# Kernel tuning notes

Hardware: AMD Instinct MI355X
Metric: run time of the kernel (lower is better)

Reference implementation:

```python
import jax, jax.numpy as jnp
import numpy as np

N = 100000          # total nodes
E = 1600000         # total edges
B = 500             # graphs in batch
NODES_PER_GRAPH = N // B
D_X, D_XDA = 96, 32
IN = D_X + D_XDA    # 128
HID = 128
OUT = 128


def setup_inputs() -> dict:
    key = jax.random.key(0)
    ks = jax.random.split(key, 12)
    s = 0.05
    x = jax.random.normal(ks[0], (N, D_X), jnp.float32)
    x_da = jax.random.normal(ks[1], (N, D_XDA), jnp.float32)
    edge_index = jax.random.randint(ks[2], (2, E), 0, N, jnp.int32).astype(jnp.int64)
    batch = (jnp.arange(N, dtype=jnp.int64) // NODES_PER_GRAPH)
    rootindex = jnp.arange(B, dtype=jnp.int64) * NODES_PER_GRAPH
    return {
        'x': x, 'x_da': x_da, 'edge_index': edge_index,
        'batch': batch, 'rootindex': rootindex,
        'td_w1': jax.random.normal(ks[3], (IN, HID), jnp.float32) * s,
        'td_b1': jnp.zeros((HID,), jnp.float32),
        'td_w2': jax.random.normal(ks[4], (HID + IN, OUT), jnp.float32) * s,
        'td_b2': jnp.zeros((OUT,), jnp.float32),
        'bu_w1': jax.random.normal(ks[5], (IN, HID), jnp.float32) * s,
        'bu_b1': jnp.zeros((HID,), jnp.float32),
        'bu_w2': jax.random.normal(ks[6], (HID + IN, OUT), jnp.float32) * s,
        'bu_b2': jnp.zeros((OUT,), jnp.float32),
        'mlp_w1': jax.random.normal(ks[7], ((OUT + HID) * 2, 2 * HID), jnp.float32) * s,
        'mlp_b1': jnp.zeros((2 * HID,), jnp.float32),
        'mlp_w2': jax.random.normal(ks[8], (2 * HID, 2), jnp.float32) * s,
        'mlp_b2': jnp.zeros((2,), jnp.float32),
    }


def gcn_conv(h, src, dst, W, b):
    # PyG GCNConv: h' = D^{-1/2} (A + I) D^{-1/2} (h W) + b,
    # messages flow src -> dst, deg counts incoming edges + self loop.
    h = h @ W                                              # [N, out]
    deg = jax.ops.segment_sum(jnp.ones((src.shape[0],), h.dtype), dst,
                              num_segments=N) + 1.0        # self loop
    dinv = jax.lax.rsqrt(deg)                              # deg >= 1
    norm = dinv[src] * dinv[dst]                           # [E]
    agg = jax.ops.segment_sum(h[src] * norm[:, None], dst, num_segments=N)
    agg = agg + h * (dinv * dinv)[:, None]                 # self-loop term
    return agg + b


def branch(x0, src, dst, w1, b1, w2, b2, batch, rootindex):
    # x0: [N, IN] = cat(x, x_da)
    x1 = x0
    h = gcn_conv(x0, src, dst, w1, b1)                     # [N, HID]
    x2 = h
    root1 = x1[rootindex[batch]]                           # root-extend gather
    h = jax.nn.relu(jnp.concatenate([h, root1], axis=1))   # dropout off (eval)
    h = jax.nn.relu(gcn_conv(h, src, dst, w2, b2))         # [N, OUT]
    root2 = x2[rootindex[batch]]
    h = jnp.concatenate([h, root2], axis=1)                # [N, OUT+HID]
    # scatter_mean over graphs
    sums = jax.ops.segment_sum(h, batch, num_segments=B)
    cnt = jax.ops.segment_sum(jnp.ones((N,), h.dtype), batch, num_segments=B)
    return sums / cnt[:, None]                             # [B, OUT+HID]


def reference(x, x_da, edge_index, batch, rootindex,
              td_w1, td_b1, td_w2, td_b2,
              bu_w1, bu_b1, bu_w2, bu_b2,
              mlp_w1, mlp_b1, mlp_w2, mlp_b2):
    x0 = jnp.concatenate([x, x_da], axis=1)                # [N, IN]
    src, dst = edge_index[0], edge_index[1]
    td = branch(x0, src, dst, td_w1, td_b1, td_w2, td_b2, batch, rootindex)
    bu = branch(x0, dst, src, bu_w1, bu_b1, bu_w2, bu_b2, batch, rootindex)
    g = jnp.concatenate([bu, td], axis=1)                  # [B, 4*HID]
    h = jax.nn.relu(g @ mlp_w1 + mlp_b1)
    return h @ mlp_w2 + mlp_b2                             # [B, 2]
```

## Files before the change

kernel.cpp:

```cpp
#include <hip/hip_runtime.h>

#define NN 100000
#define NE 1600000
#define NB 500
#define NPG 200
#define BS 128
#define NBUK 782
#define SLAB 2560
#define EPB2 4096
#define NEB2 391
#define NBLK 1563

typedef unsigned short ushortT;
typedef __attribute__((ext_vector_type(8))) short bf16x8;
typedef __attribute__((ext_vector_type(4))) float f32x4;

#define MFMA16(a, b, c) __builtin_amdgcn_mfma_f32_16x16x32_bf16(a, b, c, 0, 0, 0)

__device__ inline ushortT f2bf(float f) {
    unsigned u = __float_as_uint(f);
    return (ushortT)((u + 0x7FFF + ((u >> 16) & 1)) >> 16);
}
__device__ inline float bf2f(ushortT u) { return __uint_as_float((unsigned)u << 16); }
__device__ inline void addbf2(float& a0, float& a1, unsigned w) {
    a0 += __uint_as_float(w << 16);
    a1 += __uint_as_float(w & 0xFFFF0000u);
}
__device__ inline void addbf8(float* acc, uint4 w) {
    addbf2(acc[0], acc[1], w.x);
    addbf2(acc[2], acc[3], w.y);
    addbf2(acc[4], acc[5], w.z);
    addbf2(acc[6], acc[7], w.w);
}
__device__ inline bf16x8 cvt8(float4 f0, float4 f1) {
    bf16x8 r;
    r[0] = (short)f2bf(f0.x); r[1] = (short)f2bf(f0.y);
    r[2] = (short)f2bf(f0.z); r[3] = (short)f2bf(f0.w);
    r[4] = (short)f2bf(f1.x); r[5] = (short)f2bf(f1.y);
    r[6] = (short)f2bf(f1.z); r[7] = (short)f2bf(f1.w);
    return r;
}
__device__ inline bf16x8 relu_bf8(uint4 w) {
    bf16x8 r;
    unsigned ws[4] = {w.x, w.y, w.z, w.w};
#pragma unroll
    for (int i = 0; i < 4; i++) {
        unsigned v = ws[i];
        unsigned lo = (v & 0x8000u) ? 0u : (v & 0xFFFFu);
        unsigned hi = (v & 0x80000000u) ? 0u : (v & 0xFFFF0000u);
        r[2 * i]     = (short)lo;
        r[2 * i + 1] = (short)(hi >> 16);
    }
    return r;
}

__global__ void wprep_k(const float* __restrict__ w0, const float* __restrict__ w1,
                        const float* __restrict__ w2, const float* __restrict__ w3,
                        ushortT* __restrict__ wt) {
    int m = blockIdx.x >> 6;
    const float* w = (m == 0) ? w0 : (m == 1) ? w1 : (m == 2) ? w2 : w3;
    ushortT* o = wt + m * 16384;
    int idx = (blockIdx.x & 63) * 256 + threadIdx.x;
    int n = idx >> 7, k = idx & 127;
    o[idx] = f2bf(w[k * 128 + n]);
}

__global__ __launch_bounds__(512) void stage_slab_k(const int* __restrict__ ei,
                                                    int* __restrict__ bcnt_td,
                                                    int* __restrict__ bcnt_bu,
                                                    int* __restrict__ st_td,
                                                    int* __restrict__ st_bu) {
    __shared__ int h0[NBUK], h1[NBUK];
    const int t = threadIdx.x;
    for (int i = t; i < NBUK; i += 512) { h0[i] = 0; h1[i] = 0; }
    __syncthreads();
    int base = blockIdx.x * EPB2;
    int a[EPB2 / 512], b[EPB2 / 512];
#pragma unroll
    for (int j = 0; j < EPB2 / 512; j++) {
        int e = base + t + j * 512;
        a[j] = -1;
        if (e < NE) {
            a[j] = ei[e]; b[j] = ei[NE + e];
            atomicAdd(&h0[b[j] >> 7], 1);
            atomicAdd(&h1[a[j] >> 7], 1);
        }
    }
    __syncthreads();
    for (int i = t; i < NBUK; i += 512) {
        int c0 = h0[i], c1 = h1[i];
        if (c0) h0[i] = atomicAdd(&bcnt_td[i], c0);
        if (c1) h1[i] = atomicAdd(&bcnt_bu[i], c1);
    }
    __syncthreads();
#pragma unroll
    for (int j = 0; j < EPB2 / 512; j++) {
        if (a[j] >= 0) {
            int bk0 = b[j] >> 7;
            int o0 = atomicAdd(&h0[bk0], 1);
            st_td[bk0 * SLAB + o0] = (a[j] << 7) | (b[j] & 127);
            int bk1 = a[j] >> 7;
            int o1 = atomicAdd(&h1[bk1], 1);
            st_bu[bk1 * SLAB + o1] = (b[j] << 7) | (a[j] & 127);
        }
    }
}

__global__ __launch_bounds__(1024) void bscan_k(
    const int* __restrict__ c0, const int* __restrict__ c1,
    int* __restrict__ b0, int* __restrict__ b1) {
    const int* c = blockIdx.x ? c1 : c0;
    int* bb = blockIdx.x ? b1 : b0;
    __shared__ int sh[1024];
    const int t = threadIdx.x;
    int v = (t < NBUK) ? c[t] : 0;
    sh[t] = v;
    __syncthreads();
#pragma unroll
    for (int off = 1; off < 1024; off <<= 1) {
        int add = (t >= off) ? sh[t - off] : 0;
        __syncthreads();
        sh[t] += add;
        __syncthreads();
    }
    int excl = sh[t] - v;
    if (t < NBUK) bb[t] = excl;
    if (t == NBUK - 1) bb[NBUK] = sh[t];
}

__global__ __launch_bounds__(256) void place2_k(
    const int* __restrict__ st_td, const int* __restrict__ st_bu,
    const int* __restrict__ bcnt_td, const int* __restrict__ bcnt_bu,
    const int* __restrict__ bb_td, const int* __restrict__ bb_bu,
    int* __restrict__ rp_td, int* __restrict__ rp_bu,
    int* __restrict__ csr_td, int* __restrict__ csr_bu,
    float* __restrict__ dinv_td, float* __restrict__ dinv_bu) {
    const int dir = blockIdx.x >= NBUK;
    const int bucket = dir ? blockIdx.x - NBUK : blockIdx.x;
    const int* stage = (dir ? st_bu : st_td) + bucket * SLAB;
    const int n = (dir ? bcnt_bu : bcnt_td)[bucket];
    const int obase = (dir ? bb_bu : bb_td)[bucket];
    int* rp = dir ? rp_bu : rp_td;
    int* csr = dir ? csr_bu : csr_td;
    float* dinv = dir ? dinv_bu : dinv_td;

    const int node0 = bucket << 7;
    __shared__ int lcnt[BS], lsc[BS], lcur[BS];
    const int t = threadIdx.x;
    if (t < BS) lcnt[t] = 0;
    __syncthreads();
    for (int i = t; i < n; i += 256) atomicAdd(&lcnt[stage[i] & 127], 1);
    __syncthreads();
    if (t < BS) lsc[t] = lcnt[t];
    __syncthreads();
#pragma unroll
    for (int off = 1; off < BS; off <<= 1) {
        int add = (t < BS && t >= off) ? lsc[t - off] : 0;
        __syncthreads();
        if (t < BS) lsc[t] += add;
        __syncthreads();
    }
    if (t < BS) {
        int excl = lsc[t] - lcnt[t];
        lcur[t] = obase + excl;
        int node = node0 + t;
        if (node < NN) {
            rp[node] = obase + excl;
            dinv[node] = rsqrtf((float)(lcnt[t] + 1));
        }
    }
    if (bucket == NBUK - 1 && t == 0) rp[NN] = obase + n;
    __syncthreads();
    for (int i = t; i < n; i += 256) {
        int s = stage[i];
        int off = atomicAdd(&lcur[s & 127], 1);
        csr[off] = (int)((unsigned)s >> 7);
    }
}

__global__ __launch_bounds__(256) void gemm1x_k(
    const float* __restrict__ x, const float* __restrict__ xda,
    const ushortT* __restrict__ WTa, const ushortT* __restrict__ WTb,
    const float* __restrict__ dinv_a, const float* __restrict__ dinv_b,
    ushortT* __restrict__ hs_a, ushortT* __restrict__ hs_b) {
    const int t = threadIdx.x;
    const int wv = t >> 6, l = t & 63, lr = l & 15, lk = l >> 4;
    const int row0 = blockIdx.x * 64;
    const int cb0 = (wv * 2) * 16, cb1 = (wv * 2 + 1) * 16;

    bf16x8 bfr[2][2][4];
#pragma unroll
    for (int br = 0; br < 2; br++) {
        const ushortT* WT = br ? WTb : WTa;
#pragma unroll
        for (int c = 0; c < 2; c++) {
            const ushortT* base = WT + (size_t)((wv * 2 + c) * 16 + lr) * 128 + lk * 8;
#pragma unroll
            for (int kk = 0; kk < 4; kk++)
                bfr[br][c][kk] = *reinterpret_cast<const bf16x8*>(base + kk * 32);
        }
    }

#pragma unroll
    for (int rt = 0; rt < 4; rt++) {
        const int rtbase = row0 + rt * 16;
        int arow = rtbase + lr; if (arow >= NN) arow = NN - 1;
        bf16x8 af[4];
#pragma unroll
        for (int kk = 0; kk < 4; kk++) {
            int c8 = kk * 4 + lk;
            float4 f0, f1;
            if (c8 < 12) {
                const float* p = x + (size_t)arow * 96 + c8 * 8;
                f0 = *(const float4*)p; f1 = *(const float4*)(p + 4);
            } else {
                const float* p = xda + (size_t)arow * 32 + (c8 - 12) * 8;
                f0 = *(const float4*)p; f1 = *(const float4*)(p + 4);
            }
            af[kk] = cvt8(f0, f1);
        }
        f32x4 a00 = {0,0,0,0}, a01 = {0,0,0,0}, a10 = {0,0,0,0}, a11 = {0,0,0,0};
#pragma unroll
        for (int kk = 0; kk < 4; kk++) {
            a00 = MFMA16(af[kk], bfr[0][0][kk], a00);
            a01 = MFMA16(af[kk], bfr[0][1][kk], a01);
            a10 = MFMA16(af[kk], bfr[1][0][kk], a10);
            a11 = MFMA16(af[kk], bfr[1][1][kk], a11);
        }
        const int srow = rtbase + lk * 4;
        float4 da = *(const float4*)(dinv_a + srow);
        float4 db = *(const float4*)(dinv_b + srow);
        const float* dap = (const float*)&da;
        const float* dbp = (const float*)&db;
#pragma unroll
        for (int e = 0; e < 4; e++) {
            int r = srow + e;
            if (r < NN) {
                size_t ro = (size_t)r * 128;
                hs_a[ro + cb0 + lr] = f2bf(a00[e] * dap[e]);
                hs_a[ro + cb1 + lr] = f2bf(a01[e] * dap[e]);
                hs_b[ro + cb0 + lr] = f2bf(a10[e] * dbp[e]);
                hs_b[ro + cb1 + lr] = f2bf(a11[e] * dbp[e]);
            }
        }
    }
}

__global__ __launch_bounds__(256) void gemm2x_k(
    const ushortT* __restrict__ agg_a, const ushortT* __restrict__ agg_b,
    const ushortT* __restrict__ WTa, const ushortT* __restrict__ WTb,
    const float* __restrict__ rm_a, const float* __restrict__ rm_b,
    const float* __restrict__ dinv_a, const float* __restrict__ dinv_b,
    ushortT* __restrict__ hs_a, ushortT* __restrict__ hs_b) {
    const int brn = blockIdx.x >= NBLK;
    const ushortT* agg = brn ? agg_b : agg_a;
    const ushortT* WT  = brn ? WTb : WTa;
    const float* rm    = brn ? rm_b : rm_a;
    const float* dinv  = brn ? dinv_b : dinv_a;
    ushortT* hs        = brn ? hs_b : hs_a;
    const int blk = brn ? blockIdx.x - NBLK : blockIdx.x;
    const int t = threadIdx.x;
    const int wv = t >> 6, l = t & 63, lr = l & 15, lk = l >> 4;
    const int row0 = blk * 64;
    const int cb0 = (wv * 2) * 16, cb1 = (wv * 2 + 1) * 16;

    bf16x8 bfr[2][4];
#pragma unroll
    for (int c = 0; c < 2; c++) {
        const ushortT* base = WT + (size_t)((wv * 2 + c) * 16 + lr) * 128 + lk * 8;
#pragma unroll
        for (int kk = 0; kk < 4; kk++)
            bfr[c][kk] = *reinterpret_cast<const bf16x8*>(base + kk * 32);
    }

#pragma unroll
    for (int rt = 0; rt < 4; rt++) {
        const int rtbase = row0 + rt * 16;
        int arow = rtbase + lr; if (arow >= NN) arow = NN - 1;
        const ushortT* ap = agg + (size_t)arow * 128 + lk * 8;
        bf16x8 af[4];
#pragma unroll
        for (int kk = 0; kk < 4; kk++)
            af[kk] = relu_bf8(*reinterpret_cast<const uint4*>(ap + kk * 32));
        f32x4 a0 = {0,0,0,0}, a1 = {0,0,0,0};
#pragma unroll
        for (int kk = 0; kk < 4; kk++) {
            a0 = MFMA16(af[kk], bfr[0][kk], a0);
            a1 = MFMA16(af[kk], bfr[1][kk], a1);
        }
        const int srow = rtbase + lk * 4;
        float4 dv = *(const float4*)(dinv + srow);
        const float* dvp = (const float*)&dv;
#pragma unroll
        for (int e = 0; e < 4; e++) {
            int r = srow + e;
            if (r < NN) {
                int bg = r / NPG;
                size_t ro = (size_t)r * 128;
                float r0 = rm[(size_t)bg * 128 + cb0 + lr];
                float r1 = rm[(size_t)bg * 128 + cb1 + lr];
                hs[ro + cb0 + lr] = f2bf((a0[e] + r0) * dvp[e]);
                hs[ro + cb1 + lr] = f2bf((a1[e] + r1) * dvp[e]);
            }
        }
    }
}

template <int MODE>
__global__ __launch_bounds__(256) void gather16_k(
    const int* __restrict__ rp_a, const int* __restrict__ csr_a,
    const float* __restrict__ dinv_a, const ushortT* __restrict__ hs_a,
    const float* __restrict__ bias_a,
    const int* __restrict__ rp_b, const int* __restrict__ csr_b,
    const float* __restrict__ dinv_b, const ushortT* __restrict__ hs_b,
    const float* __restrict__ bias_b,
    ushortT* __restrict__ out_a, ushortT* __restrict__ out_b) {
    int v = blockIdx.x * 16 + (threadIdx.x >> 4);
    if (v >= NN) return;
    const int lane = threadIdx.x & 15;
    int ba = rp_a[v], ea = rp_a[v + 1];
    int bb = rp_b[v], eb = rp_b[v + 1];
    float acc_a[8], acc_b[8];
#pragma unroll
    for (int k = 0; k < 8; k++) { acc_a[k] = 0.f; acc_b[k] = 0.f; }
    addbf8(acc_a, *(const uint4*)(hs_a + (size_t)v * 128 + lane * 8));
    addbf8(acc_b, *(const uint4*)(hs_b + (size_t)v * 128 + lane * 8));

    while (ba < ea || bb < eb) {
        int na = ea - ba; if (na > 16) na = 16; if (na < 0) na = 0;
        int nb = eb - bb; if (nb > 16) nb = 16; if (nb < 0) nb = 0;
        int ia = (lane < na) ? csr_a[ba + lane] : 0;
        int ib = (lane < nb) ? csr_b[bb + lane] : 0;
#pragma unroll
        for (int i = 0; i < 16; i += 8) {
            if (i >= na && i >= nb) break;
            uint4 ua[8], ub[8];
            if (i < na) {
#pragma unroll
                for (int j = 0; j < 8; j++) {
                    int s = __shfl(ia, i + j, 16);
                    ua[j] = *(const uint4*)(hs_a + (size_t)s * 128 + lane * 8);
                }
            }
            if (i < nb) {
#pragma unroll
                for (int j = 0; j < 8; j++) {
                    int s = __shfl(ib, i + j, 16);
                    ub[j] = *(const uint4*)(hs_b + (size_t)s * 128 + lane * 8);
                }
            }
            if (i < na) {
#pragma unroll
                for (int j = 0; j < 8; j++)
                    if (i + j < na) addbf8(acc_a, ua[j]);
            }
            if (i < nb) {
#pragma unroll
                for (int j = 0; j < 8; j++)
                    if (i + j < nb) addbf8(acc_b, ub[j]);
            }
        }
        ba += 16; bb += 16;
    }

    float da = dinv_a[v], db = dinv_b[v];
    float4 pa0 = *(const float4*)(bias_a + lane * 8);
    float4 pa1 = *(const float4*)(bias_a + lane * 8 + 4);
    float4 pb0 = *(const float4*)(bias_b + lane * 8);
    float4 pb1 = *(const float4*)(bias_b + lane * 8 + 4);
    float oa[8], ob[8];
    const float* pap = (const float*)&pa0;
    oa[0] = fmaf(acc_a[0], da, pa0.x); oa[1] = fmaf(acc_a[1], da, pa0.y);
    oa[2] = fmaf(acc_a[2], da, pa0.z); oa[3] = fmaf(acc_a[3], da, pa0.w);
    oa[4] = fmaf(acc_a[4], da, pa1.x); oa[5] = fmaf(acc_a[5], da, pa1.y);
    oa[6] = fmaf(acc_a[6], da, pa1.z); oa[7] = fmaf(acc_a[7], da, pa1.w);
    ob[0] = fmaf(acc_b[0], db, pb0.x); ob[1] = fmaf(acc_b[1], db, pb0.y);
    ob[2] = fmaf(acc_b[2], db, pb0.z); ob[3] = fmaf(acc_b[3], db, pb0.w);
    ob[4] = fmaf(acc_b[4], db, pb1.x); ob[5] = fmaf(acc_b[5], db, pb1.y);
    ob[6] = fmaf(acc_b[6], db, pb1.z); ob[7] = fmaf(acc_b[7], db, pb1.w);
    (void)pap;
    if (MODE == 1) {
#pragma unroll
        for (int k = 0; k < 8; k++) { oa[k] = fmaxf(oa[k], 0.f); ob[k] = fmaxf(ob[k], 0.f); }
    }
    uint4 wa, wb;
    wa.x = (unsigned)f2bf(oa[0]) | ((unsigned)f2bf(oa[1]) << 16);
    wa.y = (unsigned)f2bf(oa[2]) | ((unsigned)f2bf(oa[3]) << 16);
    wa.z = (unsigned)f2bf(oa[4]) | ((unsigned)f2bf(oa[5]) << 16);
    wa.w = (unsigned)f2bf(oa[6]) | ((unsigned)f2bf(oa[7]) << 16);
    wb.x = (unsigned)f2bf(ob[0]) | ((unsigned)f2bf(ob[1]) << 16);
    wb.y = (unsigned)f2bf(ob[2]) | ((unsigned)f2bf(ob[3]) << 16);
    wb.z = (unsigned)f2bf(ob[4]) | ((unsigned)f2bf(ob[5]) << 16);
    wb.w = (unsigned)f2bf(ob[6]) | ((unsigned)f2bf(ob[7]) << 16);
    *(uint4*)(out_a + (size_t)v * 128 + lane * 8) = wa;
    *(uint4*)(out_b + (size_t)v * 128 + lane * 8) = wb;
}

__global__ void roots_k(
    const float* __restrict__ x, const float* __restrict__ xda,
    const int* __restrict__ root,
    const ushortT* __restrict__ agg_a, const ushortT* __restrict__ agg_b,
    const float* __restrict__ W2a, const float* __restrict__ W2b,
    float* __restrict__ x2a, float* __restrict__ x2b,
    float* __restrict__ rma, float* __restrict__ rmb) {
    __shared__ float xr[128];
    int b = blockIdx.x, t = threadIdx.x;
    int r = root[b];
    if (t < 128) {
        float val = (t < 96) ? x[(size_t)r * 96 + t] : xda[(size_t)r * 32 + (t - 96)];
        xr[t] = fmaxf(val, 0.f);
    }
    __syncthreads();
    int br = t >> 7, c = t & 127;
    const ushortT* agg = br ? agg_b : agg_a;
    const float* W2 = br ? W2b : W2a;
    float* x2 = br ? x2b : x2a;
    float* rm = br ? rmb : rma;
    x2[(size_t)b * 128 + c] = bf2f(agg[(size_t)r * 128 + c]);
    float acc = 0.f;
#pragma unroll 8
    for (int k = 0; k < 128; k++)
        acc = fmaf(xr[k], W2[(size_t)(128 + k) * 128 + c], acc);
    rm[(size_t)b * 128 + c] = acc;
}

__global__ void gmean_k(const ushortT* __restrict__ ra, const ushortT* __restrict__ rb,
                        const float* __restrict__ x2a, const float* __restrict__ x2b,
                        float* __restrict__ gbuf) {
    int b = blockIdx.x, t = threadIdx.x;
    int br = t >> 7, c = t & 127;
    const ushortT* src = br ? rb : ra;
    size_t base = (size_t)b * NPG * 128 + c;
    float s = 0.f;
#pragma unroll 4
    for (int r = 0; r < NPG; r++)
        s += bf2f(src[base + (size_t)r * 128]);
    const float* x2 = br ? x2b : x2a;
    int o = br ? 256 : 0;
    gbuf[(size_t)b * 512 + o + c] = s * (1.0f / NPG);
    gbuf[(size_t)b * 512 + o + 128 + c] = x2[(size_t)b * 128 + c];
}

__global__ void mlp_k(const float* __restrict__ g, const float* __restrict__ w1,
                      const float* __restrict__ b1, const float* __restrict__ w2,
                      const float* __restrict__ b2, float* __restrict__ out) {
    __shared__ float gs[512];
    __shared__ float parts[4][2];
    int b = blockIdx.x, t = threadIdx.x;
    gs[t] = g[(size_t)b * 512 + t];
    gs[t + 256] = g[(size_t)b * 512 + 256 + t];
    __syncthreads();
    float acc = b1[t];
#pragma unroll 8
    for (int k = 0; k < 512; k++)
        acc = fmaf(gs[k], w1[(size_t)k * 256 + t], acc);
    float hv = fmaxf(acc, 0.f);
    float p0 = hv * w2[t * 2 + 0];
    float p1 = hv * w2[t * 2 + 1];
#pragma unroll
    for (int off = 32; off; off >>= 1) {
        p0 += __shfl_down(p0, off);
        p1 += __shfl_down(p1, off);
    }
    int w = t >> 6;
    if ((t & 63) == 0) { parts[w][0] = p0; parts[w][1] = p1; }
    __syncthreads();
    if (t == 0) {
        out[b * 2 + 0] = parts[0][0] + parts[1][0] + parts[2][0] + parts[3][0] + b2[0];
        out[b * 2 + 1] = parts[0][1] + parts[1][1] + parts[2][1] + parts[3][1] + b2[1];
    }
}

extern "C" void kernel_launch(void* const* d_in, const int* in_sizes, int n_in,
                              void* d_out, int out_size, void* d_ws, size_t ws_size,
                              hipStream_t stream) {
    const float* x     = (const float*)d_in[0];
    const float* xda   = (const float*)d_in[1];
    const int*   ei    = (const int*)d_in[2];
    const int*   root  = (const int*)d_in[4];
    const float* td_w1 = (const float*)d_in[5];
    const float* td_b1 = (const float*)d_in[6];
    const float* td_w2 = (const float*)d_in[7];
    const float* td_b2 = (const float*)d_in[8];
    const float* bu_w1 = (const float*)d_in[9];
    const float* bu_b1 = (const float*)d_in[10];
    const float* bu_w2 = (const float*)d_in[11];
    const float* bu_b2 = (const float*)d_in[12];
    const float* mw1   = (const float*)d_in[13];
    const float* mb1   = (const float*)d_in[14];
    const float* mw2   = (const float*)d_in[15];
    const float* mb2   = (const float*)d_in[16];
    float* out = (float*)d_out;

    ushortT* agg_bu  = (ushortT*)d_ws;
    ushortT* agg_td  = agg_bu + (size_t)NN * 128;
    ushortT* hs_bu   = agg_td + (size_t)NN * 128;
    ushortT* hs_td   = hs_bu + (size_t)NN * 128;
    float*   dinv_td = (float*)(hs_td + (size_t)NN * 128);
    float*   dinv_bu = dinv_td + NN;
    float*   x2_bu   = dinv_bu + NN;
    float*   x2_td   = x2_bu + (size_t)NB * 128;
    float*   rm_bu   = x2_td + (size_t)NB * 128;
    float*   rm_td   = rm_bu + (size_t)NB * 128;
    float*   gbuf    = rm_td + (size_t)NB * 128;
    ushortT* wt1_bu  = (ushortT*)(gbuf + (size_t)NB * 512);
    ushortT* wt1_td  = wt1_bu + 16384;
    ushortT* wt2_bu  = wt1_td + 16384;
    ushortT* wt2_td  = wt2_bu + 16384;
    int*     bcnt_td = (int*)(wt2_td + 16384);
    int*     bcnt_bu = bcnt_td + NBUK;
    int*     bbase_td= bcnt_bu + NBUK;
    int*     bbase_bu= bbase_td + NBUK + 1;
    int*     rp_td   = bbase_bu + NBUK + 1;
    int*     rp_bu   = rp_td + NN + 1;
    int*     csr_td  = rp_bu + NN + 1;
    int*     csr_bu  = csr_td + NE;
    int*     st_td   = (int*)agg_bu;
    int*     st_bu   = st_td + NBUK * SLAB;

    hipMemsetAsync(bcnt_td, 0, (size_t)(2 * NBUK) * sizeof(int), stream);

    wprep_k<<<4 * 64, 256, 0, stream>>>(bu_w1, td_w1, bu_w2, td_w2, wt1_bu);
    stage_slab_k<<<NEB2, 512, 0, stream>>>(ei, bcnt_td, bcnt_bu, st_td, st_bu);
    bscan_k<<<2, 1024, 0, stream>>>(bcnt_td, bcnt_bu, bbase_td, bbase_bu);
    place2_k<<<2 * NBUK, 256, 0, stream>>>(st_td, st_bu, bcnt_td, bcnt_bu,
                                           bbase_td, bbase_bu,
                                           rp_td, rp_bu, csr_td, csr_bu, dinv_td, dinv_bu);

    gemm1x_k<<<NBLK, 256, 0, stream>>>(x, xda, wt1_bu, wt1_td, dinv_bu, dinv_td, hs_bu, hs_td);
    gather16_k<0><<<(NN + 15) / 16, 256, 0, stream>>>(
        rp_bu, csr_bu, dinv_bu, hs_bu, bu_b1,
        rp_td, csr_td, dinv_td, hs_td, td_b1, agg_bu, agg_td);

    roots_k<<<NB, 256, 0, stream>>>(x, xda, root, agg_bu, agg_td, bu_w2, td_w2,
                                    x2_bu, x2_td, rm_bu, rm_td);

    gemm2x_k<<<2 * NBLK, 256, 0, stream>>>(agg_bu, agg_td, wt2_bu, wt2_td,
                                           rm_bu, rm_td, dinv_bu, dinv_td, hs_bu, hs_td);
    gather16_k<1><<<(NN + 15) / 16, 256, 0, stream>>>(
        rp_bu, csr_bu, dinv_bu, hs_bu, bu_b2,
        rp_td, csr_td, dinv_td, hs_td, td_b2, agg_bu, agg_td);

    gmean_k<<<NB, 256, 0, stream>>>(agg_bu, agg_td, x2_bu, x2_td, gbuf);
    mlp_k<<<NB, 256, 0, stream>>>(gbuf, mw1, mb1, mw2, mb2, out);
}
```

Measured before the change: 475.6 us.

## Fuse edge bucketing with first GEMM, move dinv scaling into gather, fuse mean-pool

Merges the edge-staging kernel and the first-layer GEMM into one launch. Removing the dinv dependency from the GEMMs lets the GEMM overlap with CSR construction. The separate bucket scan kernel is dropped; each place block recomputes its own prefix base by summing the bucket counts before it. The gather now uses 32 lanes per node with 4-wide loads and scales each neighbour by its dinv inside the loop. The second gather folds ReLU and the per-graph mean into a shared-memory reduction plus global atomics, which removes the gmean kernel and the write-back of layer-2 activations. In exchange it does more per-edge work in the gathers, adds float atomics, and repeats the prefix sum redundantly in every place block.

```diff
diff --git a/kernel.cpp b/kernel.cpp
--- a/kernel.cpp
+++ b/kernel.cpp
@@ -7,8 +7,8 @@
 #define BS 128
 #define NBUK 782
 #define SLAB 2560
-#define EPB2 4096
-#define NEB2 391
+#define EPB3 2048
+#define NEB3 782
 #define NBLK 1563
 
 typedef unsigned short ushortT;
@@ -22,15 +22,8 @@
     return (ushortT)((u + 0x7FFF + ((u >> 16) & 1)) >> 16);
 }
 __device__ inline float bf2f(ushortT u) { return __uint_as_float((unsigned)u << 16); }
-__device__ inline void addbf2(float& a0, float& a1, unsigned w) {
-    a0 += __uint_as_float(w << 16);
-    a1 += __uint_as_float(w & 0xFFFF0000u);
-}
-__device__ inline void addbf8(float* acc, uint4 w) {
-    addbf2(acc[0], acc[1], w.x);
-    addbf2(acc[2], acc[3], w.y);
-    addbf2(acc[4], acc[5], w.z);
-    addbf2(acc[6], acc[7], w.w);
+__device__ inline float4 bf4_to_f4(ushort4 u) {
+    return make_float4(bf2f(u.x), bf2f(u.y), bf2f(u.z), bf2f(u.w));
 }
 __device__ inline bf16x8 cvt8(float4 f0, float4 f1) {
     bf16x8 r;
@@ -65,127 +58,53 @@
     o[idx] = f2bf(w[k * 128 + n]);
 }
 
-__global__ __launch_bounds__(512) void stage_slab_k(const int* __restrict__ ei,
-                                                    int* __restrict__ bcnt_td,
-                                                    int* __restrict__ bcnt_bu,
-                                                    int* __restrict__ st_td,
-                                                    int* __restrict__ st_bu) {
-    __shared__ int h0[NBUK], h1[NBUK];
-    const int t = threadIdx.x;
-    for (int i = t; i < NBUK; i += 512) { h0[i] = 0; h1[i] = 0; }
-    __syncthreads();
-    int base = blockIdx.x * EPB2;
-    int a[EPB2 / 512], b[EPB2 / 512];
-#pragma unroll
-    for (int j = 0; j < EPB2 / 512; j++) {
-        int e = base + t + j * 512;
-        a[j] = -1;
-        if (e < NE) {
-            a[j] = ei[e]; b[j] = ei[NE + e];
-            atomicAdd(&h0[b[j] >> 7], 1);
-            atomicAdd(&h1[a[j] >> 7], 1);
-        }
-    }
-    __syncthreads();
-    for (int i = t; i < NBUK; i += 512) {
-        int c0 = h0[i], c1 = h1[i];
-        if (c0) h0[i] = atomicAdd(&bcnt_td[i], c0);
-        if (c1) h1[i] = atomicAdd(&bcnt_bu[i], c1);
-    }
-    __syncthreads();
-#pragma unroll
-    for (int j = 0; j < EPB2 / 512; j++) {
-        if (a[j] >= 0) {
-            int bk0 = b[j] >> 7;
-            int o0 = atomicAdd(&h0[bk0], 1);
-            st_td[bk0 * SLAB + o0] = (a[j] << 7) | (b[j] & 127);
-            int bk1 = a[j] >> 7;
-            int o1 = atomicAdd(&h1[bk1], 1);
-            st_bu[bk1 * SLAB + o1] = (b[j] << 7) | (a[j] & 127);
-        }
-    }
-}
-
-__global__ __launch_bounds__(1024) void bscan_k(
-    const int* __restrict__ c0, const int* __restrict__ c1,
-    int* __restrict__ b0, int* __restrict__ b1) {
-    const int* c = blockIdx.x ? c1 : c0;
-    int* bb = blockIdx.x ? b1 : b0;
-    __shared__ int sh[1024];
-    const int t = threadIdx.x;
-    int v = (t < NBUK) ? c[t] : 0;
-    sh[t] = v;
-    __syncthreads();
-#pragma unroll
-    for (int off = 1; off < 1024; off <<= 1) {
-        int add = (t >= off) ? sh[t - off] : 0;
-        __syncthreads();
-        sh[t] += add;
-        __syncthreads();
-    }
-    int excl = sh[t] - v;
-    if (t < NBUK) bb[t] = excl;
-    if (t == NBUK - 1) bb[NBUK] = sh[t];
-}
-
-__global__ __launch_bounds__(256) void place2_k(
-    const int* __restrict__ st_td, const int* __restrict__ st_bu,
-    const int* __restrict__ bcnt_td, const int* __restrict__ bcnt_bu,
-    const int* __restrict__ bb_td, const int* __restrict__ bb_bu,
-    int* __restrict__ rp_td, int* __restrict__ rp_bu,
-    int* __restrict__ csr_td, int* __restrict__ csr_bu,
-    float* __restrict__ dinv_td, float* __restrict__ dinv_bu) {
-    const int dir = blockIdx.x >= NBUK;
-    const int bucket = dir ? blockIdx.x - NBUK : blockIdx.x;
-    const int* stage = (dir ? st_bu : st_td) + bucket * SLAB;
-    const int n = (dir ? bcnt_bu : bcnt_td)[bucket];
-    const int obase = (dir ? bb_bu : bb_td)[bucket];
-    int* rp = dir ? rp_bu : rp_td;
-    int* csr = dir ? csr_bu : csr_td;
-    float* dinv = dir ? dinv_bu : dinv_td;
-
-    const int node0 = bucket << 7;
-    __shared__ int lcnt[BS], lsc[BS], lcur[BS];
-    const int t = threadIdx.x;
-    if (t < BS) lcnt[t] = 0;
-    __syncthreads();
-    for (int i = t; i < n; i += 256) atomicAdd(&lcnt[stage[i] & 127], 1);
-    __syncthreads();
-    if (t < BS) lsc[t] = lcnt[t];
-    __syncthreads();
-#pragma unroll
-    for (int off = 1; off < BS; off <<= 1) {
-        int add = (t < BS && t >= off) ? lsc[t - off] : 0;
-        __syncthreads();
-        if (t < BS) lsc[t] += add;
-        __syncthreads();
-    }
-    if (t < BS) {
-        int excl = lsc[t] - lcnt[t];
-        lcur[t] = obase + excl;
-        int node = node0 + t;
-        if (node < NN) {
-            rp[node] = obase + excl;
-            dinv[node] = rsqrtf((float)(lcnt[t] + 1));
-        }
-    }
-    if (bucket == NBUK - 1 && t == 0) rp[NN] = obase + n;
-    __syncthreads();
-    for (int i = t; i < n; i += 256) {
-        int s = stage[i];
-        int off = atomicAdd(&lcur[s & 127], 1);
-        csr[off] = (int)((unsigned)s >> 7);
-    }
-}
-
-__global__ __launch_bounds__(256) void gemm1x_k(
+__global__ __launch_bounds__(256) void phase1_k(
+    const int* __restrict__ ei,
+    int* __restrict__ bcnt_td, int* __restrict__ bcnt_bu,
+    int* __restrict__ st_td, int* __restrict__ st_bu,
     const float* __restrict__ x, const float* __restrict__ xda,
     const ushortT* __restrict__ WTa, const ushortT* __restrict__ WTb,
-    const float* __restrict__ dinv_a, const float* __restrict__ dinv_b,
     ushortT* __restrict__ hs_a, ushortT* __restrict__ hs_b) {
     const int t = threadIdx.x;
+    if (blockIdx.x < NEB3) {
+        __shared__ int h0[NBUK], h1[NBUK];
+        for (int i = t; i < NBUK; i += 256) { h0[i] = 0; h1[i] = 0; }
+        __syncthreads();
+        int base = blockIdx.x * EPB3;
+        int a[8], b[8];
+#pragma unroll
+        for (int j = 0; j < 8; j++) {
+            int e = base + t + j * 256;
+            a[j] = -1;
+            if (e < NE) {
+                a[j] = ei[e]; b[j] = ei[NE + e];
+                atomicAdd(&h0[b[j] >> 7], 1);
+                atomicAdd(&h1[a[j] >> 7], 1);
+            }
+        }
+        __syncthreads();
+        for (int i = t; i < NBUK; i += 256) {
+            int c0 = h0[i], c1 = h1[i];
+            if (c0) h0[i] = atomicAdd(&bcnt_td[i], c0);
+            if (c1) h1[i] = atomicAdd(&bcnt_bu[i], c1);
+        }
+        __syncthreads();
+#pragma unroll
+        for (int j = 0; j < 8; j++) {
+            if (a[j] >= 0) {
+                int bk0 = b[j] >> 7;
+                int o0 = atomicAdd(&h0[bk0], 1);
+                st_td[bk0 * SLAB + o0] = (a[j] << 7) | (b[j] & 127);
+                int bk1 = a[j] >> 7;
+                int o1 = atomicAdd(&h1[bk1], 1);
+                st_bu[bk1 * SLAB + o1] = (b[j] << 7) | (a[j] & 127);
+            }
+        }
+        return;
+    }
+    const int blk = blockIdx.x - NEB3;
     const int wv = t >> 6, l = t & 63, lr = l & 15, lk = l >> 4;
-    const int row0 = blockIdx.x * 64;
+    const int row0 = blk * 64;
     const int cb0 = (wv * 2) * 16, cb1 = (wv * 2 + 1) * 16;
 
     bf16x8 bfr[2][2][4];
@@ -228,21 +147,78 @@
             a11 = MFMA16(af[kk], bfr[1][1][kk], a11);
         }
         const int srow = rtbase + lk * 4;
-        float4 da = *(const float4*)(dinv_a + srow);
-        float4 db = *(const float4*)(dinv_b + srow);
-        const float* dap = (const float*)&da;
-        const float* dbp = (const float*)&db;
 #pragma unroll
         for (int e = 0; e < 4; e++) {
             int r = srow + e;
             if (r < NN) {
                 size_t ro = (size_t)r * 128;
-                hs_a[ro + cb0 + lr] = f2bf(a00[e] * dap[e]);
-                hs_a[ro + cb1 + lr] = f2bf(a01[e] * dap[e]);
-                hs_b[ro + cb0 + lr] = f2bf(a10[e] * dbp[e]);
-                hs_b[ro + cb1 + lr] = f2bf(a11[e] * dbp[e]);
-            }
-        }
+                hs_a[ro + cb0 + lr] = f2bf(a00[e]);
+                hs_a[ro + cb1 + lr] = f2bf(a01[e]);
+                hs_b[ro + cb0 + lr] = f2bf(a10[e]);
+                hs_b[ro + cb1 + lr] = f2bf(a11[e]);
+            }
+        }
+    }
+}
+
+__global__ __launch_bounds__(256) void place2_k(
+    const int* __restrict__ st_td, const int* __restrict__ st_bu,
+    const int* __restrict__ bcnt_td, const int* __restrict__ bcnt_bu,
+    int* __restrict__ rp_td, int* __restrict__ rp_bu,
+    int* __restrict__ csr_td, int* __restrict__ csr_bu,
+    float* __restrict__ dinv_td, float* __restrict__ dinv_bu) {
+    const int dir = blockIdx.x >= NBUK;
+    const int bucket = dir ? blockIdx.x - NBUK : blockIdx.x;
+    const int* stage = (dir ? st_bu : st_td) + bucket * SLAB;
+    const int* bcnt = dir ? bcnt_bu : bcnt_td;
+    const int n = bcnt[bucket];
+    int* rp = dir ? rp_bu : rp_td;
+    int* csr = dir ? csr_bu : csr_td;
+    float* dinv = dir ? dinv_bu : dinv_td;
+    const int t = threadIdx.x;
+
+    __shared__ int rw[4];
+    __shared__ int sh_obase;
+    int part = 0;
+    for (int i = t; i < bucket; i += 256) part += bcnt[i];
+#pragma unroll
+    for (int off = 32; off; off >>= 1) part += __shfl_down(part, off);
+    if ((t & 63) == 0) rw[t >> 6] = part;
+    __syncthreads();
+    if (t == 0) sh_obase = rw[0] + rw[1] + rw[2] + rw[3];
+    __syncthreads();
+    const int obase = sh_obase;
+
+    const int node0 = bucket << 7;
+    __shared__ int lcnt[BS], lsc[BS], lcur[BS];
+    if (t < BS) lcnt[t] = 0;
+    __syncthreads();
+    for (int i = t; i < n; i += 256) atomicAdd(&lcnt[stage[i] & 127], 1);
+    __syncthreads();
+    if (t < BS) lsc[t] = lcnt[t];
+    __syncthreads();
+#pragma unroll
+    for (int off = 1; off < BS; off <<= 1) {
+        int add = (t < BS && t >= off) ? lsc[t - off] : 0;
+        __syncthreads();
+        if (t < BS) lsc[t] += add;
+        __syncthreads();
+    }
+    if (t < BS) {
+        int excl = lsc[t] - lcnt[t];
+        lcur[t] = obase + excl;
+        int node = node0 + t;
+        if (node < NN) {
+            rp[node] = obase + excl;
+            dinv[node] = rsqrtf((float)(lcnt[t] + 1));
+        }
+    }
+    if (bucket == NBUK - 1 && t == 0) rp[NN] = obase + n;
+    __syncthreads();
+    for (int i = t; i < n; i += 256) {
+        int s = stage[i];
+        int off = atomicAdd(&lcur[s & 127], 1);
+        csr[off] = (int)((unsigned)s >> 7);
     }
 }
 
@@ -250,13 +226,11 @@
     const ushortT* __restrict__ agg_a, const ushortT* __restrict__ agg_b,
     const ushortT* __restrict__ WTa, const ushortT* __restrict__ WTb,
     const float* __restrict__ rm_a, const float* __restrict__ rm_b,
-    const float* __restrict__ dinv_a, const float* __restrict__ dinv_b,
     ushortT* __restrict__ hs_a, ushortT* __restrict__ hs_b) {
     const int brn = blockIdx.x >= NBLK;
     const ushortT* agg = brn ? agg_b : agg_a;
     const ushortT* WT  = brn ? WTb : WTa;
     const float* rm    = brn ? rm_b : rm_a;
-    const float* dinv  = brn ? dinv_b : dinv_a;
     ushortT* hs        = brn ? hs_b : hs_a;
     const int blk = brn ? blockIdx.x - NBLK : blockIdx.x;
     const int t = threadIdx.x;
@@ -289,8 +263,6 @@
             a1 = MFMA16(af[kk], bfr[1][kk], a1);
         }
         const int srow = rtbase + lk * 4;
-        float4 dv = *(const float4*)(dinv + srow);
-        const float* dvp = (const float*)&dv;
 #pragma unroll
         for (int e = 0; e < 4; e++) {
             int r = srow + e;
@@ -299,101 +271,119 @@
                 size_t ro = (size_t)r * 128;
                 float r0 = rm[(size_t)bg * 128 + cb0 + lr];
                 float r1 = rm[(size_t)bg * 128 + cb1 + lr];
-                hs[ro + cb0 + lr] = f2bf((a0[e] + r0) * dvp[e]);
-                hs[ro + cb1 + lr] = f2bf((a1[e] + r1) * dvp[e]);
+                hs[ro + cb0 + lr] = f2bf(a0[e] + r0);
+                hs[ro + cb1 + lr] = f2bf(a1[e] + r1);
             }
         }
     }
 }
 
 template <int MODE>
-__global__ __launch_bounds__(256) void gather16_k(
+__global__ __launch_bounds__(256) void gather32_k(
     const int* __restrict__ rp_a, const int* __restrict__ csr_a,
     const float* __restrict__ dinv_a, const ushortT* __restrict__ hs_a,
     const float* __restrict__ bias_a,
     const int* __restrict__ rp_b, const int* __restrict__ csr_b,
     const float* __restrict__ dinv_b, const ushortT* __restrict__ hs_b,
     const float* __restrict__ bias_b,
-    ushortT* __restrict__ out_a, ushortT* __restrict__ out_b) {
-    int v = blockIdx.x * 16 + (threadIdx.x >> 4);
-    if (v >= NN) return;
-    const int lane = threadIdx.x & 15;
+    ushortT* __restrict__ out_a, ushortT* __restrict__ out_b,
+    float* __restrict__ gbuf) {
+    const int t = threadIdx.x;
+    const int v = blockIdx.x * 8 + (t >> 5);
+    const int lane = t & 31;
+    __shared__ float sacc[256];
+    if (MODE == 1) { sacc[t] = 0.f; __syncthreads(); }
+
     int ba = rp_a[v], ea = rp_a[v + 1];
     int bb = rp_b[v], eb = rp_b[v + 1];
-    float acc_a[8], acc_b[8];
-#pragma unroll
-    for (int k = 0; k < 8; k++) { acc_a[k] = 0.f; acc_b[k] = 0.f; }
-    addbf8(acc_a, *(const uint4*)(hs_a + (size_t)v * 128 + lane * 8));
-    addbf8(acc_b, *(const uint4*)(hs_b + (size_t)v * 128 + lane * 8));
+    float dva = dinv_a[v], dvb = dinv_b[v];
+    float4 fs = bf4_to_f4(((const ushort4*)(hs_a + (size_t)v * 128))[lane]);
+    float4 acc_a = make_float4(fs.x * dva, fs.y * dva, fs.z * dva, fs.w * dva);
+    fs = bf4_to_f4(((const ushort4*)(hs_b + (size_t)v * 128))[lane]);
+    float4 acc_b = make_float4(fs.x * dvb, fs.y * dvb, fs.z * dvb, fs.w * dvb);
 
     while (ba < ea || bb < eb) {
-        int na = ea - ba; if (na > 16) na = 16; if (na < 0) na = 0;
-        int nb = eb - bb; if (nb > 16) nb = 16; if (nb < 0) nb = 0;
+        int na = ea - ba; if (na > 32) na = 32; if (na < 0) na = 0;
+        int nb = eb - bb; if (nb > 32) nb = 32; if (nb < 0) nb = 0;
         int ia = (lane < na) ? csr_a[ba + lane] : 0;
         int ib = (lane < nb) ? csr_b[bb + lane] : 0;
-#pragma unroll
-        for (int i = 0; i < 16; i += 8) {
+        float fa = dinv_a[ia];
+        float fb = dinv_b[ib];
+        for (int i = 0; i < 32; i += 8) {
             if (i >= na && i >= nb) break;
-            uint4 ua[8], ub[8];
+            ushort4 ua[8], ub[8];
+            float da8[8], db8[8];
             if (i < na) {
 #pragma unroll
                 for (int j = 0; j < 8; j++) {
-                    int s = __shfl(ia, i + j, 16);
-                    ua[j] = *(const uint4*)(hs_a + (size_t)s * 128 + lane * 8);
+                    int s = __shfl(ia, i + j, 32);
+                    da8[j] = __shfl(fa, i + j, 32);
+                    ua[j] = ((const ushort4*)(hs_a + (size_t)s * 128))[lane];
                 }
             }
             if (i < nb) {
 #pragma unroll
                 for (int j = 0; j < 8; j++) {
-                    int s = __shfl(ib, i + j, 16);
-                    ub[j] = *(const uint4*)(hs_b + (size_t)s * 128 + lane * 8);
+                    int s = __shfl(ib, i + j, 32);
+                    db8[j] = __shfl(fb, i + j, 32);
+                    ub[j] = ((const ushort4*)(hs_b + (size_t)s * 128))[lane];
                 }
             }
             if (i < na) {
 #pragma unroll
                 for (int j = 0; j < 8; j++)
-                    if (i + j < na) addbf8(acc_a, ua[j]);
+                    if (i + j < na) {
+                        float4 f = bf4_to_f4(ua[j]);
+                        acc_a.x = fmaf(f.x, da8[j], acc_a.x);
+                        acc_a.y = fmaf(f.y, da8[j], acc_a.y);
+                        acc_a.z = fmaf(f.z, da8[j], acc_a.z);
+                        acc_a.w = fmaf(f.w, da8[j], acc_a.w);
+                    }
             }
             if (i < nb) {
 #pragma unroll
                 for (int j = 0; j < 8; j++)
-                    if (i + j < nb) addbf8(acc_b, ub[j]);
-            }
-        }
-        ba += 16; bb += 16;
-    }
-
-    float da = dinv_a[v], db = dinv_b[v];
-    float4 pa0 = *(const float4*)(bias_a + lane * 8);
-    float4 pa1 = *(const float4*)(bias_a + lane * 8 + 4);
-    float4 pb0 = *(const float4*)(bias_b + lane * 8);
-    float4 pb1 = *(const float4*)(bias_b + lane * 8 + 4);
-    float oa[8], ob[8];
-    const float* pap = (const float*)&pa0;
-    oa[0] = fmaf(acc_a[0], da, pa0.x); oa[1] = fmaf(acc_a[1], da, pa0.y);
-    oa[2] = fmaf(acc_a[2], da, pa0.z); oa[3] = fmaf(acc_a[3], da, pa0.w);
-    oa[4] = fmaf(acc_a[4], da, pa1.x); oa[5] = fmaf(acc_a[5], da, pa1.y);
-    oa[6] = fmaf(acc_a[6], da, pa1.z); oa[7] = fmaf(acc_a[7], da, pa1.w);
-    ob[0] = fmaf(acc_b[0], db, pb0.x); ob[1] = fmaf(acc_b[1], db, pb0.y);
-    ob[2] = fmaf(acc_b[2], db, pb0.z); ob[3] = fmaf(acc_b[3], db, pb0.w);
-    ob[4] = fmaf(acc_b[4], db, pb1.x); ob[5] = fmaf(acc_b[5], db, pb1.y);
-    ob[6] = fmaf(acc_b[6], db, pb1.z); ob[7] = fmaf(acc_b[7], db, pb1.w);
-    (void)pap;
-    if (MODE == 1) {
-#pragma unroll
-        for (int k = 0; k < 8; k++) { oa[k] = fmaxf(oa[k], 0.f); ob[k] = fmaxf(ob[k], 0.f); }
-    }
-    uint4 wa, wb;
-    wa.x = (unsigned)f2bf(oa[0]) | ((unsigned)f2bf(oa[1]) << 16);
-    wa.y = (unsigned)f2bf(oa[2]) | ((unsigned)f2bf(oa[3]) << 16);
-    wa.z = (unsigned)f2bf(oa[4]) | ((unsigned)f2bf(oa[5]) << 16);
-    wa.w = (unsigned)f2bf(oa[6]) | ((unsigned)f2bf(oa[7]) << 16);
-    wb.x = (unsigned)f2bf(ob[0]) | ((unsigned)f2bf(ob[1]) << 16);
-    wb.y = (unsigned)f2bf(ob[2]) | ((unsigned)f2bf(ob[3]) << 16);
-    wb.z = (unsigned)f2bf(ob[4]) | ((unsigned)f2bf(ob[5]) << 16);
-    wb.w = (unsigned)f2bf(ob[6]) | ((unsigned)f2bf(ob[7]) << 16);
-    *(uint4*)(out_a + (size_t)v * 128 + lane * 8) = wa;
-    *(uint4*)(out_b + (size_t)v * 128 + lane * 8) = wb;
+                    if (i + j < nb) {
+                        float4 f = bf4_to_f4(ub[j]);
+                        acc_b.x = fmaf(f.x, db8[j], acc_b.x);
+                        acc_b.y = fmaf(f.y, db8[j], acc_b.y);
+                        acc_b.z = fmaf(f.z, db8[j], acc_b.z);
+                        acc_b.w = fmaf(f.w, db8[j], acc_b.w);
+                    }
+            }
+        }
+        ba += 32; bb += 32;
+    }
+
+    float4 pa = ((const float4*)bias_a)[lane];
+    float4 pb = ((const float4*)bias_b)[lane];
+    float4 oa = make_float4(fmaf(acc_a.x, dva, pa.x), fmaf(acc_a.y, dva, pa.y),
+                            fmaf(acc_a.z, dva, pa.z), fmaf(acc_a.w, dva, pa.w));
+    float4 ob = make_float4(fmaf(acc_b.x, dvb, pb.x), fmaf(acc_b.y, dvb, pb.y),
+                            fmaf(acc_b.z, dvb, pb.z), fmaf(acc_b.w, dvb, pb.w));
+    if (MODE == 0) {
+        ((ushort4*)(out_a + (size_t)v * 128))[lane] =
+            make_ushort4(f2bf(oa.x), f2bf(oa.y), f2bf(oa.z), f2bf(oa.w));
+        ((ushort4*)(out_b + (size_t)v * 128))[lane] =
+            make_ushort4(f2bf(ob.x), f2bf(ob.y), f2bf(ob.z), f2bf(ob.w));
+    } else {
+        const float sc = 1.0f / NPG;
+        oa.x = fmaxf(oa.x, 0.f) * sc; oa.y = fmaxf(oa.y, 0.f) * sc;
+        oa.z = fmaxf(oa.z, 0.f) * sc; oa.w = fmaxf(oa.w, 0.f) * sc;
+        ob.x = fmaxf(ob.x, 0.f) * sc; ob.y = fmaxf(ob.y, 0.f) * sc;
+        ob.z = fmaxf(ob.z, 0.f) * sc; ob.w = fmaxf(ob.w, 0.f) * sc;
+        atomicAdd(&sacc[lane * 4 + 0], oa.x);
+        atomicAdd(&sacc[lane * 4 + 1], oa.y);
+        atomicAdd(&sacc[lane * 4 + 2], oa.z);
+        atomicAdd(&sacc[lane * 4 + 3], oa.w);
+        atomicAdd(&sacc[128 + lane * 4 + 0], ob.x);
+        atomicAdd(&sacc[128 + lane * 4 + 1], ob.y);
+        atomicAdd(&sacc[128 + lane * 4 + 2], ob.z);
+        atomicAdd(&sacc[128 + lane * 4 + 3], ob.w);
+        __syncthreads();
+        int g = (blockIdx.x * 8) / NPG;
+        unsafeAtomicAdd(&gbuf[(size_t)g * 256 + t], sacc[t]);
+    }
 }
 
 __global__ void roots_k(
@@ -424,31 +414,18 @@
     rm[(size_t)b * 128 + c] = acc;
 }
 
-__global__ void gmean_k(const ushortT* __restrict__ ra, const ushortT* __restrict__ rb,
-                        const float* __restrict__ x2a, const float* __restrict__ x2b,
-                        float* __restrict__ gbuf) {
-    int b = blockIdx.x, t = threadIdx.x;
-    int br = t >> 7, c = t & 127;
-    const ushortT* src = br ? rb : ra;
-    size_t base = (size_t)b * NPG * 128 + c;
-    float s = 0.f;
-#pragma unroll 4
-    for (int r = 0; r < NPG; r++)
-        s += bf2f(src[base + (size_t)r * 128]);
-    const float* x2 = br ? x2b : x2a;
-    int o = br ? 256 : 0;
-    gbuf[(size_t)b * 512 + o + c] = s * (1.0f / NPG);
-    gbuf[(size_t)b * 512 + o + 128 + c] = x2[(size_t)b * 128 + c];
-}
-
-__global__ void mlp_k(const float* __restrict__ g, const float* __restrict__ w1,
-                      const float* __restrict__ b1, const float* __restrict__ w2,
-                      const float* __restrict__ b2, float* __restrict__ out) {
+__global__ void mlp_k(const float* __restrict__ gbuf,
+                      const float* __restrict__ x2a, const float* __restrict__ x2b,
+                      const float* __restrict__ w1, const float* __restrict__ b1,
+                      const float* __restrict__ w2, const float* __restrict__ b2,
+                      float* __restrict__ out) {
     __shared__ float gs[512];
     __shared__ float parts[4][2];
     int b = blockIdx.x, t = threadIdx.x;
-    gs[t] = g[(size_t)b * 512 + t];
-    gs[t + 256] = g[(size_t)b * 512 + 256 + t];
+    gs[t]       = (t < 128) ? gbuf[(size_t)b * 256 + t]
+                            : x2a[(size_t)b * 128 + (t - 128)];
+    gs[256 + t] = (t < 128) ? gbuf[(size_t)b * 256 + 128 + t]
+                            : x2b[(size_t)b * 128 + (t - 128)];
     __syncthreads();
     float acc = b1[t];
 #pragma unroll 8
@@ -503,15 +480,13 @@
     float*   rm_bu   = x2_td + (size_t)NB * 128;
     float*   rm_td   = rm_bu + (size_t)NB * 128;
     float*   gbuf    = rm_td + (size_t)NB * 128;
-    ushortT* wt1_bu  = (ushortT*)(gbuf + (size_t)NB * 512);
+    ushortT* wt1_bu  = (ushortT*)(gbuf + (size_t)NB * 256);
     ushortT* wt1_td  = wt1_bu + 16384;
     ushortT* wt2_bu  = wt1_td + 16384;
     ushortT* wt2_td  = wt2_bu + 16384;
     int*     bcnt_td = (int*)(wt2_td + 16384);
     int*     bcnt_bu = bcnt_td + NBUK;
-    int*     bbase_td= bcnt_bu + NBUK;
-    int*     bbase_bu= bbase_td + NBUK + 1;
-    int*     rp_td   = bbase_bu + NBUK + 1;
+    int*     rp_td   = bcnt_bu + NBUK;
     int*     rp_bu   = rp_td + NN + 1;
     int*     csr_td  = rp_bu + NN + 1;
     int*     csr_bu  = csr_td + NE;
@@ -519,28 +494,28 @@
     int*     st_bu   = st_td + NBUK * SLAB;
 
     hipMemsetAsync(bcnt_td, 0, (size_t)(2 * NBUK) * sizeof(int), stream);
+    hipMemsetAsync(gbuf, 0, (size_t)NB * 256 * sizeof(float), stream);
 
     wprep_k<<<4 * 64, 256, 0, stream>>>(bu_w1, td_w1, bu_w2, td_w2, wt1_bu);
-    stage_slab_k<<<NEB2, 512, 0, stream>>>(ei, bcnt_td, bcnt_bu, st_td, st_bu);
-    bscan_k<<<2, 1024, 0, stream>>>(bcnt_td, bcnt_bu, bbase_td, bbase_bu);
+
+    phase1_k<<<NEB3 + NBLK, 256, 0, stream>>>(ei, bcnt_td, bcnt_bu, st_td, st_bu,
+                                              x, xda, wt1_bu, wt1_td, hs_bu, hs_td);
     place2_k<<<2 * NBUK, 256, 0, stream>>>(st_td, st_bu, bcnt_td, bcnt_bu,
-                                           bbase_td, bbase_bu,
                                            rp_td, rp_bu, csr_td, csr_bu, dinv_td, dinv_bu);
 
-    gemm1x_k<<<NBLK, 256, 0, stream>>>(x, xda, wt1_bu, wt1_td, dinv_bu, dinv_td, hs_bu, hs_td);
-    gather16_k<0><<<(NN + 15) / 16, 256, 0, stream>>>(
+    gather32_k<0><<<NN / 8, 256, 0, stream>>>(
         rp_bu, csr_bu, dinv_bu, hs_bu, bu_b1,
-        rp_td, csr_td, dinv_td, hs_td, td_b1, agg_bu, agg_td);
+        rp_td, csr_td, dinv_td, hs_td, td_b1, agg_bu, agg_td, nullptr);
 
     roots_k<<<NB, 256, 0, stream>>>(x, xda, root, agg_bu, agg_td, bu_w2, td_w2,
                                     x2_bu, x2_td, rm_bu, rm_td);
 
     gemm2x_k<<<2 * NBLK, 256, 0, stream>>>(agg_bu, agg_td, wt2_bu, wt2_td,
-                                           rm_bu, rm_td, dinv_bu, dinv_td, hs_bu, hs_td);
-    gather16_k<1><<<(NN + 15) / 16, 256, 0, stream>>>(
+                                           rm_bu, rm_td, hs_bu, hs_td);
+
+    gather32_k<1><<<NN / 8, 256, 0, stream>>>(
         rp_bu, csr_bu, dinv_bu, hs_bu, bu_b2,
-        rp_td, csr_td, dinv_td, hs_td, td_b2, agg_bu, agg_td);
-
-    gmean_k<<<NB, 256, 0, stream>>>(agg_bu, agg_td, x2_bu, x2_td, gbuf);
-    mlp_k<<<NB, 256, 0, stream>>>(gbuf, mw1, mb1, mw2, mb2, out);
-}
+        rp_td, csr_td, dinv_td, hs_td, td_b2, nullptr, nullptr, gbuf);
+
+    mlp_k<<<NB, 256, 0, stream>>>(gbuf, x2_bu, x2_td, mw1, mb1, mw2, mb2, out);
+}
```

Result: slower. 542.0 us (+14.0%).
